# Kernel optimization log

Measured on AMD Instinct MI355X. Metric: run time of the kernel, lower is better.

## Reference

```python
import jax, jax.numpy as jnp
import numpy as np

N = 200000          # num_particles
E = 6400000         # num edges (avg degree 32)
ENV = 3             # env_dim
HIST = 15           # hist_v feature dim (5 steps * env_dim)
RADIUS = 0.05
VEL_MEAN = 0.0
VEL_STD = 1.0


def setup_inputs() -> dict:
    key = jax.random.key(0)
    k1, k2, k3, k4 = jax.random.split(key, 4)
    pos = jax.random.uniform(k1, (N, ENV), dtype=jnp.float32)
    hist_v = jax.random.normal(k2, (N, HIST), dtype=jnp.float32)
    src = jax.random.randint(k3, (E,), 0, N, dtype=jnp.int32)
    # offset in [1, N-1] guarantees no self-loops (rel_pos != 0)
    off = jax.random.randint(k4, (E,), 1, N, dtype=jnp.int32)
    dst = (src + off) % N
    boundary_info = jnp.array([0.0, 1.0, 0.0, 1.0, 0.0, 1.0], dtype=jnp.float32)
    return {"pos": pos, "hist_v": hist_v, "boundary_info": boundary_info,
            "src": src, "dst": dst}


def reference(pos, hist_v, boundary_info, src, dst):
    # node features
    current_v = hist_v[:, :ENV]                                  # [N, 3]
    normalized_v = (hist_v - VEL_MEAN) / VEL_STD                 # [N, 15]
    # pos repeat_interleave(2, dim=1): [x,x,y,y,z,z] minus per-dim lo/hi bounds
    pos2bound = jnp.repeat(pos, 2, axis=1) - boundary_info[None, :]  # [N, 6]
    normalized_pos2bound = jnp.clip(pos2bound / RADIUS, -1.0, 1.0)
    node_feature = jnp.concatenate([normalized_v, normalized_pos2bound], axis=1)  # [N, 21]

    # edge features: u_sub_v gather-subtract over edges
    rel_pos = (pos[src] - pos[dst]) / RADIUS                     # [E, 3]
    rel_dis = jnp.linalg.norm(rel_pos, axis=1, keepdims=True)    # [E, 1]
    edge_feature = jnp.concatenate([rel_pos, rel_dis], axis=1)   # [E, 4]

    return (node_feature.astype(jnp.float32),
            edge_feature.astype(jnp.float32),
            current_v.astype(jnp.float32))
```

## Files before the change

### kernel.cpp

```cpp
#include <hip/hip_runtime.h>
#include <math.h>


static constexpr float INV_R = 20.0f;

typedef float f32x4 __attribute__((ext_vector_type(4)));
typedef int   i32x4 __attribute__((ext_vector_type(4)));
typedef float f32x2 __attribute__((ext_vector_type(2), aligned(4)));

__global__ __launch_bounds__(256) void fused_kernel(
    const float* __restrict__ pos,
    const float* __restrict__ hist_v,
    const float* __restrict__ bnd,
    const i32x4* __restrict__ src4,
    const i32x4* __restrict__ dst4,
    float* __restrict__ node_feat,
    f32x4* __restrict__ edge_feat,
    float* __restrict__ cur_v,
    int n, int e4, int node_blocks)
{
    if ((int)blockIdx.x < node_blocks) {
        const int stride = node_blocks * blockDim.x;
        const int tid = blockIdx.x * blockDim.x + threadIdx.x;

        const int total_nf = n * 21;
        for (int idx = tid; idx < total_nf; idx += stride) {
            const int node = idx / 21;
            const int c = idx - node * 21;
            float v;
            if (c < 15) {
                v = hist_v[node * 15 + c];
            } else {
                const int j = c - 15;
                const float p = pos[node * 3 + (j >> 1)];
                v = (p - bnd[j]) * INV_R;
                v = fminf(1.0f, fmaxf(-1.0f, v));
            }
            node_feat[idx] = v;
        }

        const int total_cv = n * 3;
        for (int idx = tid; idx < total_cv; idx += stride) {
            const int node = idx / 3;
            const int c = idx - node * 3;
            cur_v[idx] = hist_v[node * 15 + c];
        }
    } else {
        const int t = (blockIdx.x - node_blocks) * blockDim.x + threadIdx.x;
        if (t >= e4) return;

        const i32x4 s4 = src4[t];
        const i32x4 d4 = dst4[t];

        float sx[4], sy[4], sz[4], dx[4], dy[4], dz[4];
#pragma unroll
        for (int k = 0; k < 4; ++k) {
            const float* ps = pos + (size_t)s4[k] * 3;
            const float* pd = pos + (size_t)d4[k] * 3;
            const f32x2 sxy = *(const f32x2*)ps;
            const float szv = ps[2];
            const f32x2 dxy = *(const f32x2*)pd;
            const float dzv = pd[2];
            sx[k] = sxy.x; sy[k] = sxy.y; sz[k] = szv;
            dx[k] = dxy.x; dy[k] = dxy.y; dz[k] = dzv;
        }
#pragma unroll
        for (int k = 0; k < 4; ++k) {
            const float rx = (sx[k] - dx[k]) * INV_R;
            const float ry = (sy[k] - dy[k]) * INV_R;
            const float rz = (sz[k] - dz[k]) * INV_R;
            const float dis = sqrtf(rx * rx + ry * ry + rz * rz);
            f32x4 o = {rx, ry, rz, dis};
            __builtin_nontemporal_store(o, &edge_feat[4 * t + k]);
        }
    }
}

extern "C" void kernel_launch(void* const* d_in, const int* in_sizes, int n_in,
                              void* d_out, int out_size, void* d_ws, size_t ws_size,
                              hipStream_t stream) {
    const float* pos    = (const float*)d_in[0];
    const float* hist_v = (const float*)d_in[1];
    const float* bnd    = (const float*)d_in[2];
    const int*   src    = (const int*)d_in[3];
    const int*   dst    = (const int*)d_in[4];

    const int N = in_sizes[0] / 3;
    const int E = in_sizes[3];
    const int e4 = E / 4;

    float* out       = (float*)d_out;
    float* node_feat = out;
    float* edge_feat = out + (size_t)N * 21;
    float* cur_v     = out + (size_t)N * 21 + (size_t)E * 4;

    const int block = 256;
    const int node_blocks = 1024;
    const int edge_blocks = (e4 + block - 1) / block;

    fused_kernel<<<node_blocks + edge_blocks, block, 0, stream>>>(
        pos, hist_v, bnd, (const i32x4*)src, (const i32x4*)dst,
        node_feat, (f32x4*)edge_feat, cur_v, N, e4, node_blocks);
}
```

Before: 243.9 us.

## Pack positions into float4 workspace for single-load edge gathers

Adds a pre-pass kernel that repacks the xyz positions into a padded float4 array in workspace. The edge kernel can then fetch each endpoint with one 16-byte aligned load instead of a split 8-byte plus 4-byte access, which cuts gather instructions and keeps each gather within one cache line. It also switches the edge output from nontemporal stores to normal stores. The cost is an extra kernel launch, an extra pass that reads and writes the position array, and a gathered footprint that grows from 12 to 16 bytes per node.

New measurement: 253.5 us. +3.9%, slower.

```diff
diff --git a/kernel.cpp b/kernel.cpp
--- a/kernel.cpp
+++ b/kernel.cpp
@@ -6,9 +6,22 @@
 
 typedef float f32x4 __attribute__((ext_vector_type(4)));
 typedef int   i32x4 __attribute__((ext_vector_type(4)));
-typedef float f32x2 __attribute__((ext_vector_type(2), aligned(4)));
+
+__global__ __launch_bounds__(256) void pack_pos_kernel(
+    const float* __restrict__ pos, f32x4* __restrict__ pos4, int n)
+{
+    const int i = blockIdx.x * blockDim.x + threadIdx.x;
+    if (i < n) {
+        const float x = pos[3 * i + 0];
+        const float y = pos[3 * i + 1];
+        const float z = pos[3 * i + 2];
+        f32x4 p = {x, y, z, 0.0f};
+        pos4[i] = p;
+    }
+}
 
 __global__ __launch_bounds__(256) void fused_kernel(
+    const f32x4* __restrict__ pos4,
     const float* __restrict__ pos,
     const float* __restrict__ hist_v,
     const float* __restrict__ bnd,
@@ -52,26 +65,20 @@
         const i32x4 s4 = src4[t];
         const i32x4 d4 = dst4[t];
 
-        float sx[4], sy[4], sz[4], dx[4], dy[4], dz[4];
+        f32x4 ps[4], pd[4];
 #pragma unroll
         for (int k = 0; k < 4; ++k) {
-            const float* ps = pos + (size_t)s4[k] * 3;
-            const float* pd = pos + (size_t)d4[k] * 3;
-            const f32x2 sxy = *(const f32x2*)ps;
-            const float szv = ps[2];
-            const f32x2 dxy = *(const f32x2*)pd;
-            const float dzv = pd[2];
-            sx[k] = sxy.x; sy[k] = sxy.y; sz[k] = szv;
-            dx[k] = dxy.x; dy[k] = dxy.y; dz[k] = dzv;
+            ps[k] = pos4[s4[k]];
+            pd[k] = pos4[d4[k]];
         }
 #pragma unroll
         for (int k = 0; k < 4; ++k) {
-            const float rx = (sx[k] - dx[k]) * INV_R;
-            const float ry = (sy[k] - dy[k]) * INV_R;
-            const float rz = (sz[k] - dz[k]) * INV_R;
+            const float rx = (ps[k].x - pd[k].x) * INV_R;
+            const float ry = (ps[k].y - pd[k].y) * INV_R;
+            const float rz = (ps[k].z - pd[k].z) * INV_R;
             const float dis = sqrtf(rx * rx + ry * ry + rz * rz);
             f32x4 o = {rx, ry, rz, dis};
-            __builtin_nontemporal_store(o, &edge_feat[4 * t + k]);
+            edge_feat[4 * t + k] = o;
         }
     }
 }
@@ -94,11 +101,16 @@
     float* edge_feat = out + (size_t)N * 21;
     float* cur_v     = out + (size_t)N * 21 + (size_t)E * 4;
 
+    f32x4* pos4 = (f32x4*)d_ws;
+
     const int block = 256;
+
+    pack_pos_kernel<<<(N + block - 1) / block, block, 0, stream>>>(pos, pos4, N);
+
     const int node_blocks = 1024;
     const int edge_blocks = (e4 + block - 1) / block;
 
     fused_kernel<<<node_blocks + edge_blocks, block, 0, stream>>>(
-        pos, hist_v, bnd, (const i32x4*)src, (const i32x4*)dst,
+        pos4, pos, hist_v, bnd, (const i32x4*)src, (const i32x4*)dst,
         node_feat, (f32x4*)edge_feat, cur_v, N, e4, node_blocks);
 }
```
